# Performance work log

Hardware: AMD Instinct MI355X
Metric: run time of the kernel (lower is better)

Reference implementation:

```python
import jax, jax.numpy as jnp
import numpy as np

NQ = 4096
N0, N1 = 32768, 8192
N = N0 + N1
F = 128          # emb_dim (32x0e+32x1e)
H = 4            # num_heads
HD = F // H
NB = 64          # fc_neurons[0] radial basis size
DEG = 32
CUTOFFS = jnp.array([2.0, 4.0], dtype=jnp.float32)
OFFSETS = jnp.array([0.1, 0.2], dtype=jnp.float32)


def _sph_harm(u):
    # component-normalized real spherical harmonics l=0,1,2 of unit vectors u [E,3]
    x, y, z = u[:, 0], u[:, 1], u[:, 2]
    s3, s15, s5 = 3.0 ** 0.5, 15.0 ** 0.5, 5.0 ** 0.5
    return jnp.stack([
        jnp.ones_like(x),
        s3 * x, s3 * y, s3 * z,
        s15 * x * y, s15 * y * z, 0.5 * s5 * (3.0 * z * z - 1.0),
        s15 * x * z, 0.5 * s15 * (x * x - y * y),
    ], axis=-1)  # [E,9]


def setup_inputs() -> dict:
    key = jax.random.key(0)
    ks = jax.random.split(key, 20)
    E0 = NQ * DEG
    E1 = NQ * DEG
    edge_src = jnp.concatenate([
        jax.random.randint(ks[0], (E0,), 0, N0),
        jax.random.randint(ks[1], (E1,), N0, N),
    ])
    edge_dst = jnp.concatenate([
        jax.random.randint(ks[2], (E0,), 0, NQ),
        jax.random.randint(ks[3], (E1,), 0, NQ),
    ])
    scale_id = jnp.concatenate([jnp.zeros((E0,), jnp.int32), jnp.ones((E1,), jnp.int32)])
    r = lambda k, sh, s=1.0: jax.random.normal(k, sh, jnp.float32) * s
    return {
        'query_coord': r(ks[4], (NQ, 3)),
        'node_feature': r(ks[5], (N, F)),
        'node_coord': r(ks[6], (N, 3)),
        'edge_src': edge_src, 'edge_dst': edge_dst, 'scale_id': scale_id,
        'b_dst': r(ks[7], (F,)),
        'Wq': r(ks[8], (F, F), F ** -0.5),
        'Wk': r(ks[9], (F, F), F ** -0.5),
        'Wv': r(ks[10], (F, F), F ** -0.5),
        'Wo': r(ks[11], (F, F), F ** -0.5),
        'bo': r(ks[12], (F,)),
        'W_rad0': r(ks[13], (NB, NB), NB ** -0.5), 'b_rad0': r(ks[14], (NB,)),
        'W_rad1': r(ks[15], (NB, NB), NB ** -0.5), 'b_rad1': r(ks[16], (NB,)),
        'W_msg': r(ks[17], (NB, F), NB ** -0.5),
        'W_sh': r(ks[18], (9, F), 9 ** -0.5),
        'W_alpha': r(ks[19], (NB, H), NB ** -0.5),
    }


def _forward(query_coord, node_feature, node_coord, b_dst, Wq, Wk, Wv, Wo, bo,
             W_rad0, b_rad0, W_rad1, b_rad1, W_msg, W_sh, W_alpha,
             edge_src, edge_dst, scale_id):
    Nq = query_coord.shape[0]
    vec = node_coord[edge_src] - query_coord[edge_dst]            # [E,3]
    rlen = jnp.sqrt(jnp.sum(vec * vec, -1) + 1e-12)               # [E]
    off = OFFSETS[scale_id]
    cut = CUTOFFS[scale_id]
    xn = (rlen - off) / (cut - off)                               # normalized radius per scale
    centers = jnp.linspace(0.0, 1.0, NB)
    std = 1.0 / NB
    g = jnp.exp(-0.5 * ((xn[:, None] - centers) / std) ** 2)      # [E,NB] gaussian RBF
    soft = 0.5 * (1.0 + jnp.cos(jnp.pi * jnp.clip((xn - 0.8) / 0.2, 0.0, 1.0)))
    g = g * soft[:, None]                                         # soft finite cutoff
    # per-scale Linear after radial basis (2 scales, masked select)
    edge_scalar = jnp.where((scale_id == 0)[:, None], g @ W_rad0 + b_rad0, g @ W_rad1 + b_rad1)
    sh = _sph_harm(vec / rlen[:, None])                           # [E,9]
    # attention GNN (equiformer-style): dst features start as zeros + learned bias
    q = (b_dst @ Wq).reshape(H, HD)
    k = (node_feature @ Wk)[edge_src].reshape(-1, H, HD)
    logits = jnp.einsum('hd,ehd->eh', q, k) / (HD ** 0.5) + edge_scalar @ W_alpha  # [E,H]
    m = jax.ops.segment_max(logits, edge_dst, num_segments=Nq)
    p = jnp.exp(logits - m[edge_dst])
    denom = jax.ops.segment_sum(p, edge_dst, num_segments=Nq)
    alpha = p / (denom[edge_dst] + 1e-9)                          # segment softmax [E,H]
    v_e = (node_feature @ Wv)[edge_src] * (edge_scalar @ W_msg) + sh @ W_sh  # [E,F]
    msg = (alpha[:, :, None] * v_e.reshape(-1, H, HD)).reshape(-1, F)
    out = jax.ops.segment_sum(msg, edge_dst, num_segments=Nq)     # [Nq,F]
    return out @ Wo + bo


def reference(query_coord, node_feature, node_coord, edge_src, edge_dst, scale_id,
              b_dst, Wq, Wk, Wv, Wo, bo, W_rad0, b_rad0, W_rad1, b_rad1,
              W_msg, W_sh, W_alpha):
    return _forward(query_coord, node_feature, node_coord, b_dst, Wq, Wk, Wv, Wo, bo,
                    W_rad0, b_rad0, W_rad1, b_rad1, W_msg, W_sh, W_alpha,
                    edge_src, edge_dst, scale_id)
```

## Files before the change

### kernel.cpp

```cpp
#include <hip/hip_runtime.h>
#include <hip/hip_bf16.h>
#include <math.h>

#define PI_F 3.14159265358979323846f

typedef __attribute__((ext_vector_type(8))) short short8v;
typedef __attribute__((ext_vector_type(4))) float f32x4;

__device__ __forceinline__ short f2bf(float x) {
    return __builtin_bit_cast(short, __float2bfloat16(x));
}
__device__ __forceinline__ float bf2f(unsigned short u) {
    return __uint_as_float(((unsigned)u) << 16);
}
__device__ __forceinline__ int pack_bf2(float a, float b) {
    return (int)(unsigned short)f2bf(a) | ((int)(unsigned short)f2bf(b) << 16);
}

static const size_t WS_WA     = 0;
static const size_t WS_BA     = 512;
static const size_t WS_BM     = 520;
static const size_t WS_WMF    = 776;
static const size_t WS_WSHF   = 8968;
static const size_t WS_QKF    = 11016;
static const size_t WS_WVF    = 12040;
static const size_t WS_WOF    = 20232;
static const size_t WS_COUNTS = 28424;
static const size_t WS_OFFS   = 36624;
static const size_t WS_CURSOR = 44824;
static const size_t WS_PACKED = 53016;
static const size_t WS_LK     = 315160;
static const size_t WS_EDP    = 479000;
static const size_t WS_EDG    = 1527576;
static const size_t WS_VB     = 2576152;
static const size_t WS_OUTPRE = 5197592;

__global__ __launch_bounds__(256) void k_prepfmt(
    const float* b_dst, const float* Wq, const float* Wk,
    const float* W_rad0, const float* b_rad0,
    const float* W_rad1, const float* b_rad1,
    const float* W_msg, const float* W_alpha, const float* Wv,
    const float* Wo, const float* W_sh,
    const int* edge_dst, const int* scale_id,
    float* Wa, float* ba, float* bm,
    short* WmF, short* WshF, short* QKF, short* WVF, short* WOF,
    int* counts, int E, int NQr) {
    __shared__ float qs_s[128];
    __shared__ float qk_s[512];
    int t = threadIdx.x;
    int b = blockIdx.x;
    if (b == 0) {
        if (t < 128) {
            float acc = 0.f;
            for (int c = 0; c < 128; ++c) acc += b_dst[c] * Wq[c * 128 + t];
            qs_s[t] = acc;
        }
        __syncthreads();
        if (t < 128) {
            const float invs = 0.17677669529663687f;
            for (int h = 0; h < 4; ++h) {
                float acc = 0.f;
                for (int d = 0; d < 32; ++d)
                    acc += Wk[t * 128 + h * 32 + d] * qs_s[h * 32 + d];
                qk_s[t * 4 + h] = acc * invs;
            }
        }
        for (int idx = t; idx < 512; idx += 256) {
            int s = idx >> 8, i = (idx >> 2) & 63, h = idx & 3;
            const float* Wr = s ? W_rad1 : W_rad0;
            float acc = 0.f;
            for (int u = 0; u < 64; ++u) acc += Wr[i * 64 + u] * W_alpha[u * 4 + h];
            Wa[idx] = acc;
        }
        if (t < 8) {
            int s = t >> 2, h = t & 3;
            const float* br = s ? b_rad1 : b_rad0;
            float acc = 0.f;
            for (int u = 0; u < 64; ++u) acc += br[u] * W_alpha[u * 4 + h];
            ba[t] = acc;
        }
        {
            int s = t >> 7, c = t & 127;
            const float* br = s ? b_rad1 : b_rad0;
            float acc = 0.f;
            for (int u = 0; u < 64; ++u) acc += br[u] * W_msg[u * 128 + c];
            bm[t] = acc;
        }
        __syncthreads();
        for (int idx = t; idx < 2048; idx += 256) {
            int j = idx & 7, lane = (idx >> 3) & 63, kh = idx >> 9;
            int k = kh * 32 + ((lane >> 4) << 3) + j;
            int col = lane & 15;
            QKF[idx] = f2bf(col < 4 ? qk_s[k * 4 + col] : 0.f);
        }
    } else if (b <= 208) {
        int item = (b - 1) * 256 + t;
        if (item < 16384) {
            int j = item & 7, lane = (item >> 3) & 63, kh = (item >> 9) & 1;
            int ct = (item >> 10) & 7, sid = item >> 13;
            int k = kh * 32 + ((lane >> 4) << 3) + j;
            int c = (lane & 15) * 8 + ct;
            const float* Wr = sid ? W_rad1 : W_rad0;
            float acc = 0.f;
            for (int u = 0; u < 64; ++u) acc += Wr[k * 64 + u] * W_msg[u * 128 + c];
            WmF[item] = f2bf(acc);
        } else if (item < 20480) {
            int i2 = item - 16384;
            int j = i2 & 7, lane = (i2 >> 3) & 63, ct = (i2 >> 9) & 7;
            int k = ((lane >> 4) << 3) + j;
            int c = (lane & 15) * 8 + ct;
            WshF[i2] = f2bf(k < 9 ? W_sh[k * 128 + c] : 0.f);
        } else if (item < 36864) {
            int i2 = item - 20480;
            int j = i2 & 7, lane = (i2 >> 3) & 63, ct = (i2 >> 9) & 7, kh = (i2 >> 12) & 3;
            int k = kh * 32 + ((lane >> 4) << 3) + j;
            int c = (lane & 15) * 8 + ct;
            WVF[i2] = f2bf(Wv[k * 128 + c]);
        } else {
            int i2 = item - 36864;
            int j = i2 & 7, lane = (i2 >> 3) & 63, ct = (i2 >> 9) & 7, kh = (i2 >> 12) & 3;
            int k = kh * 32 + ((lane >> 4) << 3) + j;
            int c = (lane & 15) * 8 + ct;
            WOF[i2] = f2bf(Wo[k * 128 + c]);
        }
    } else {
        int e = (b - 209) * 256 + t;
        if (e < E) atomicAdd(&counts[scale_id[e] * NQr + edge_dst[e]], 1);
    }
}

template <typename OUT, bool LK>
__global__ __launch_bounds__(256) void k_mgemm(
    const float* A, const short* WF, const float* bias, OUT* out,
    float* lk, const short* QKF, int M) {
    int t = threadIdx.x;
    int w = t >> 6, lane = t & 63;
    int m = lane & 15, grp = lane >> 4;
    int row0 = (blockIdx.x * 4 + w) * 16;
    if (row0 >= M) return;

    short8v a[4];
#pragma unroll
    for (int kh = 0; kh < 4; ++kh) {
        const float* ap = &A[(size_t)(row0 + m) * 128 + kh * 32 + grp * 8];
        float4 f0 = *(const float4*)ap;
        float4 f1 = *(const float4*)(ap + 4);
        a[kh][0] = f2bf(f0.x); a[kh][1] = f2bf(f0.y);
        a[kh][2] = f2bf(f0.z); a[kh][3] = f2bf(f0.w);
        a[kh][4] = f2bf(f1.x); a[kh][5] = f2bf(f1.y);
        a[kh][6] = f2bf(f1.z); a[kh][7] = f2bf(f1.w);
    }
    if constexpr (LK) {
        f32x4 cl = {0.f, 0.f, 0.f, 0.f};
#pragma unroll
        for (int kh = 0; kh < 4; ++kh) {
            short8v qb = *(const short8v*)&QKF[(kh * 64 + lane) * 8];
            cl = __builtin_amdgcn_mfma_f32_16x16x32_bf16(a[kh], qb, cl, 0, 0, 0);
        }
        if (m < 4) {
#pragma unroll
            for (int r = 0; r < 4; ++r)
                lk[(size_t)(row0 + grp * 4 + r) * 4 + m] = cl[r];
        }
    }
    f32x4 c8[8];
#pragma unroll
    for (int ct = 0; ct < 8; ++ct) {
        f32x4 c = {0.f, 0.f, 0.f, 0.f};
#pragma unroll
        for (int kh = 0; kh < 4; ++kh) {
            short8v bf = *(const short8v*)&WF[((kh * 8 + ct) * 64 + lane) * 8];
            c = __builtin_amdgcn_mfma_f32_16x16x32_bf16(a[kh], bf, c, 0, 0, 0);
        }
        c8[ct] = c;
    }
    if constexpr (sizeof(OUT) == 2) {
#pragma unroll
        for (int r = 0; r < 4; ++r) {
            int row = row0 + grp * 4 + r;
            int4 sv;
            sv.x = pack_bf2(c8[0][r], c8[1][r]);
            sv.y = pack_bf2(c8[2][r], c8[3][r]);
            sv.z = pack_bf2(c8[4][r], c8[5][r]);
            sv.w = pack_bf2(c8[6][r], c8[7][r]);
            *(int4*)&out[(size_t)row * 128 + m * 8] = sv;
        }
    } else {
        float4 b0 = make_float4(0.f, 0.f, 0.f, 0.f), b1 = b0;
        if (bias) {
            b0 = *(const float4*)&bias[m * 8];
            b1 = *(const float4*)&bias[m * 8 + 4];
        }
#pragma unroll
        for (int r = 0; r < 4; ++r) {
            int row = row0 + grp * 4 + r;
            float4 o0 = make_float4(c8[0][r] + b0.x, c8[1][r] + b0.y,
                                    c8[2][r] + b0.z, c8[3][r] + b0.w);
            float4 o1 = make_float4(c8[4][r] + b1.x, c8[5][r] + b1.y,
                                    c8[6][r] + b1.z, c8[7][r] + b1.w);
            *(float4*)&out[(size_t)row * 128 + m * 8] = o0;
            *(float4*)&out[(size_t)row * 128 + m * 8 + 4] = o1;
        }
    }
}

__global__ void k_scan(const int* counts, int* offsets, int* cursor, int nkey) {
    __shared__ int sdata[256];
    int t = threadIdx.x;
    int chunk = (nkey + 255) / 256;
    int sum = 0;
    for (int i = 0; i < chunk; ++i) {
        int idx = t * chunk + i;
        sum += (idx < nkey) ? counts[idx] : 0;
    }
    sdata[t] = sum;
    __syncthreads();
    for (int off = 1; off < 256; off <<= 1) {
        int v = (t >= off) ? sdata[t - off] : 0;
        __syncthreads();
        sdata[t] += v;
        __syncthreads();
    }
    int run = sdata[t] - sum;
    for (int i = 0; i < chunk; ++i) {
        int idx = t * chunk + i;
        if (idx < nkey) {
            offsets[idx] = run;
            cursor[idx] = run;
            run += counts[idx];
        }
    }
    if (t == 255) offsets[nkey] = sdata[255];
}

__global__ __launch_bounds__(256) void k_scatter_edge(
    const int* edge_src, const int* edge_dst, const int* scale_id,
    const float* qc, const float* nc, const float* lk,
    const float* WaB, const float* baB, int* cursor,
    int* packed, float* edP, float* edG, int E, int NQr) {
    __shared__ float WaS[512];
    __shared__ float baS[8];
    int t = threadIdx.x;
    for (int i = t; i < 512; i += 256) WaS[i] = WaB[i];
    if (t < 8) baS[t] = baB[t];
    __syncthreads();
    int e = blockIdx.x * 256 + t;
    if (e >= E) return;
    int src = edge_src[e], dst = edge_dst[e], sid = scale_id[e];
    int pos = atomicAdd(&cursor[sid * NQr + dst], 1);

    float qx = qc[dst * 3 + 0], qy = qc[dst * 3 + 1], qz = qc[dst * 3 + 2];
    float vx = nc[src * 3 + 0] - qx;
    float vy = nc[src * 3 + 1] - qy;
    float vz = nc[src * 3 + 2] - qz;
    float r = sqrtf(vx * vx + vy * vy + vz * vz + 1e-12f);
    float rinv = 1.0f / r;
    float ux = vx * rinv, uy = vy * rinv, uz = vz * rinv;

    float roff = sid ? 0.2f : 0.1f;
    float rdiv = sid ? (1.0f / 3.8f) : (1.0f / 1.9f);
    float xn = (r - roff) * rdiv;
    float su = fminf(fmaxf((xn - 0.8f) * 5.0f, 0.0f), 1.0f);
    float soft = 0.5f * (1.0f + __cosf(PI_F * su));

    float4 lkv = *(const float4*)&lk[(size_t)src * 4];

    const float qs = 64.f / 63.f;
    const float Qc = __expf(-qs * qs);
    const float* Wrow = WaS + sid * 256;
    float a0 = 0.f, a1 = 0.f, a2 = 0.f, a3 = 0.f;
#pragma unroll
    for (int ch = 0; ch < 8; ++ch) {
        float d = (xn - (float)(ch * 8) * (1.0f / 63.0f)) * 64.0f;
        float g = __expf(-0.5f * d * d);
        float tt = __expf(fminf(qs * d - 0.5f * qs * qs, 60.f));
#pragma unroll
        for (int j = 0; j < 8; ++j) {
            float4 wa = *(const float4*)&Wrow[(ch * 8 + j) * 4];
            a0 = fmaf(g, wa.x, a0);
            a1 = fmaf(g, wa.y, a1);
            a2 = fmaf(g, wa.z, a2);
            a3 = fmaf(g, wa.w, a3);
            g *= tt; tt *= Qc;
        }
    }
    float p0 = __expf(lkv.x + soft * a0 + baS[sid * 4 + 0]);
    float p1 = __expf(lkv.y + soft * a1 + baS[sid * 4 + 1]);
    float p2 = __expf(lkv.z + soft * a2 + baS[sid * 4 + 2]);
    float p3 = __expf(lkv.w + soft * a3 + baS[sid * 4 + 3]);
    packed[pos] = src | (dst << 16);
    *(float4*)&edP[(size_t)pos * 4] = make_float4(p0, p1, p2, p3);
    *(float4*)&edG[(size_t)pos * 4] = make_float4(ux, uy, uz, xn);
}

__device__ __forceinline__ short8v gchain(float xn, int k0, float soft, float Qc) {
    const float qs = 64.f / 63.f;
    float d = (xn - (float)k0 * (1.0f / 63.0f)) * 64.0f;
    float g = __expf(-0.5f * d * d);
    float tt = __expf(fminf(qs * d - 0.5f * qs * qs, 60.f));
    short8v rr;
#pragma unroll
    for (int j = 0; j < 8; ++j) {
        rr[j] = f2bf(g * soft);
        g *= tt; tt *= Qc;
    }
    return rr;
}

__global__ __launch_bounds__(256) void k_main10(
    const int* offsets, const int* packed, const float* edP, const float* edG,
    const unsigned short* Vu, const float* bm, const short* WmF, const short* WshF,
    float* out_pre, int NQr) {
    __shared__ float part[4][132];
    int t = threadIdx.x;
    int w = t >> 6, lane = t & 63;
    int sid = w & 1;
    int dst = blockIdx.x * 2 + (w >> 1);
    int m = lane & 15, grp = lane >> 4;
    int h = m >> 2;

    int key = sid * NQr + dst;
    int s0 = offsets[key], s1 = offsets[key + 1];
    int nt = (s1 - s0 + 15) >> 4;

    float acc[8];
#pragma unroll
    for (int i = 0; i < 8; ++i) acc[i] = 0.f;
    float den = 0.f;

    float4 bm0 = *(const float4*)&bm[sid * 128 + m * 8];
    float4 bm1 = *(const float4*)&bm[sid * 128 + m * 8 + 4];
    float bmv[8] = {bm0.x, bm0.y, bm0.z, bm0.w, bm1.x, bm1.y, bm1.z, bm1.w};
    const short* wmp = WmF + sid * 8192;

    const float qs = 64.f / 63.f;
    const float Qc = __expf(-qs * qs);
    const float s3 = 1.7320508075688772f, s15 = 3.872983346207417f, s5 = 2.23606797749979f;

    if (nt > 0) {
        auto loadA = [&](int tl, int (&srcs)[4], float (&ph)[4], float4& G4) {
            int q0 = s0 + tl * 16;
            int posA = q0 + m; if (posA >= s1) posA = s1 - 1;
            G4 = *(const float4*)&edG[(size_t)posA * 4];
#pragma unroll
            for (int r = 0; r < 4; ++r) {
                int pos = q0 + grp * 4 + r;
                bool valid = pos < s1;
                if (!valid) pos = s1 - 1;
                srcs[r] = packed[pos] & 0xFFFF;
                float p = edP[(size_t)pos * 4 + h];
                ph[r] = valid ? p : 0.f;
            }
        };
        auto loadV = [&](const int (&srcs)[4], int4 (&vv)[4]) {
#pragma unroll
            for (int r = 0; r < 4; ++r)
                vv[r] = *(const int4*)&Vu[(size_t)srcs[r] * 128 + m * 8];
        };

        int srcsA[4], srcsB[4], srcsC[4];
        float phA[4], phB[4], phC[4];
        float4 gA, gB, gC;
        int4 vA[4], vB[4];

        loadA(0, srcsA, phA, gA);
        loadV(srcsA, vA);
        if (nt > 1) loadA(1, srcsB, phB, gB);

        for (int tl = 0; tl < nt; ++tl) {
            if (tl + 1 < nt) loadV(srcsB, vB);
            if (tl + 2 < nt) loadA(tl + 2, srcsC, phC, gC);

            int wds[4][4];
#pragma unroll
            for (int r = 0; r < 4; ++r) {
                wds[r][0] = vA[r].x; wds[r][1] = vA[r].y;
                wds[r][2] = vA[r].z; wds[r][3] = vA[r].w;
            }
            den += phA[0] + phA[1] + phA[2] + phA[3];

            float xn = gA.w;
            float su = fminf(fmaxf((xn - 0.8f) * 5.0f, 0.0f), 1.0f);
            float soft = 0.5f * (1.0f + __cosf(PI_F * su));
            short8v aG0 = gchain(xn, grp * 8, soft, Qc);
            short8v aG1 = gchain(xn, 32 + grp * 8, soft, Qc);

            float ux = gA.x, uy = gA.y, uz = gA.z;
            float sh[9];
            sh[0] = 1.f; sh[1] = s3 * ux; sh[2] = s3 * uy; sh[3] = s3 * uz;
            sh[4] = s15 * ux * uy; sh[5] = s15 * uy * uz;
            sh[6] = 0.5f * s5 * (3.f * uz * uz - 1.f);
            sh[7] = s15 * ux * uz; sh[8] = 0.5f * s15 * (ux * ux - uy * uy);
            short8v aS;
#pragma unroll
            for (int j = 0; j < 8; ++j) {
                float v = (grp == 0) ? sh[j] : ((grp == 1 && j == 0) ? sh[8] : 0.f);
                aS[j] = f2bf(v);
            }

#pragma unroll
            for (int ct = 0; ct < 8; ++ct) {
                short8v b0 = *(const short8v*)&wmp[((ct * 2 + 0) * 64 + lane) * 8];
                short8v b1 = *(const short8v*)&wmp[((ct * 2 + 1) * 64 + lane) * 8];
                short8v bS = *(const short8v*)&WshF[(ct * 64 + lane) * 8];
                f32x4 cms = {bmv[ct], bmv[ct], bmv[ct], bmv[ct]};
                cms = __builtin_amdgcn_mfma_f32_16x16x32_bf16(aG0, b0, cms, 0, 0, 0);
                cms = __builtin_amdgcn_mfma_f32_16x16x32_bf16(aG1, b1, cms, 0, 0, 0);
                f32x4 csh = {0.f, 0.f, 0.f, 0.f};
                csh = __builtin_amdgcn_mfma_f32_16x16x32_bf16(aS, bS, csh, 0, 0, 0);
#pragma unroll
                for (int r = 0; r < 4; ++r) {
                    int wd = wds[r][ct >> 1];
                    unsigned short vu = (ct & 1) ? (unsigned short)(wd >> 16)
                                                 : (unsigned short)(wd & 0xFFFF);
                    float vf = bf2f(vu);
                    float ve = fmaf(vf, cms[r], csh[r]);
                    acc[ct] = fmaf(phA[r], ve, acc[ct]);
                }
            }

            gA = gB; gB = gC;
#pragma unroll
            for (int r = 0; r < 4; ++r) {
                phA[r] = phB[r]; phB[r] = phC[r];
                srcsB[r] = srcsC[r];
                vA[r] = vB[r];
            }
        }
    }

#pragma unroll
    for (int i = 0; i < 8; ++i) {
        acc[i] += __shfl_xor(acc[i], 16);
        acc[i] += __shfl_xor(acc[i], 32);
    }
    den += __shfl_xor(den, 16);
    den += __shfl_xor(den, 32);
    if (lane < 16) {
#pragma unroll
        for (int ct = 0; ct < 8; ++ct) part[w][m * 8 + ct] = acc[ct];
        if ((m & 3) == 0) part[w][128 + h] = den;
    }
    __syncthreads();

    {
        int which = t >> 7;
        int col = t & 127;
        int d2 = blockIdx.x * 2 + which;
        if (d2 < NQr) {
            int hh = col >> 5;
            float s = part[2 * which][col] + part[2 * which + 1][col];
            float d = part[2 * which][128 + hh] + part[2 * which + 1][128 + hh];
            out_pre[(size_t)d2 * 128 + col] = s / (d + 1e-9f);
        }
    }
}

extern "C" void kernel_launch(void* const* d_in, const int* in_sizes, int n_in,
                              void* d_out, int out_size, void* d_ws, size_t ws_size,
                              hipStream_t stream) {
    const float* query_coord = (const float*)d_in[0];
    const float* node_feature = (const float*)d_in[1];
    const float* node_coord = (const float*)d_in[2];
    const int* edge_src = (const int*)d_in[3];
    const int* edge_dst = (const int*)d_in[4];
    const int* scale_id = (const int*)d_in[5];
    const float* b_dst = (const float*)d_in[6];
    const float* Wq = (const float*)d_in[7];
    const float* Wk = (const float*)d_in[8];
    const float* Wv = (const float*)d_in[9];
    const float* Wo = (const float*)d_in[10];
    const float* bo = (const float*)d_in[11];
    const float* W_rad0 = (const float*)d_in[12];
    const float* b_rad0 = (const float*)d_in[13];
    const float* W_rad1 = (const float*)d_in[14];
    const float* b_rad1 = (const float*)d_in[15];
    const float* W_msg = (const float*)d_in[16];
    const float* W_sh = (const float*)d_in[17];
    const float* W_alpha = (const float*)d_in[18];
    (void)n_in; (void)ws_size; (void)out_size;

    int NQr = in_sizes[0] / 3;
    int Nn = in_sizes[1] / 128;
    int E = in_sizes[3];
    int nkey = NQr * 2;

    float* ws = (float*)d_ws;
    float* Wa = ws + WS_WA;
    float* ba = ws + WS_BA;
    float* bm = ws + WS_BM;
    short* WmF = (short*)(ws + WS_WMF);
    short* WshF = (short*)(ws + WS_WSHF);
    short* QKF = (short*)(ws + WS_QKF);
    short* WVF = (short*)(ws + WS_WVF);
    short* WOF = (short*)(ws + WS_WOF);
    int* counts = (int*)(ws + WS_COUNTS);
    int* offsets = (int*)(ws + WS_OFFS);
    int* cursor = (int*)(ws + WS_CURSOR);
    int* packed = (int*)(ws + WS_PACKED);
    float* lk = ws + WS_LK;
    float* edP = ws + WS_EDP;
    float* edG = ws + WS_EDG;
    unsigned short* Vb = (unsigned short*)(ws + WS_VB);
    float* out_pre = ws + WS_OUTPRE;
    float* out = (float*)d_out;

    hipMemsetAsync(counts, 0, nkey * sizeof(int), stream);
    int histBlocks = (E + 255) / 256;
    hipLaunchKernelGGL(k_prepfmt, dim3(209 + histBlocks), dim3(256), 0, stream,
                       b_dst, Wq, Wk, W_rad0, b_rad0, W_rad1, b_rad1, W_msg, W_alpha,
                       Wv, Wo, W_sh, edge_dst, scale_id,
                       Wa, ba, bm, WmF, WshF, QKF, WVF, WOF, counts, E, NQr);
    hipLaunchKernelGGL((k_mgemm<unsigned short, true>), dim3((Nn + 63) / 64), dim3(256), 0,
                       stream, node_feature, WVF, (const float*)nullptr, Vb, lk, QKF, Nn);
    hipLaunchKernelGGL(k_scan, dim3(1), dim3(256), 0, stream, counts, offsets, cursor, nkey);
    hipLaunchKernelGGL(k_scatter_edge, dim3((E + 255) / 256), dim3(256), 0, stream,
                       edge_src, edge_dst, scale_id, query_coord, node_coord, lk,
                       Wa, ba, cursor, packed, edP, edG, E, NQr);
    hipLaunchKernelGGL(k_main10, dim3((NQr + 1) / 2), dim3(256), 0, stream,
                       offsets, packed, edP, edG, Vb, bm, WmF, WshF, out_pre, NQr);
    hipLaunchKernelGGL((k_mgemm<float, false>), dim3((NQr + 63) / 64), dim3(256), 0, stream,
                       out_pre, WOF, bo, out, (float*)nullptr, (const short*)nullptr, NQr);
}
```

Baseline: 129.7 us.

## Fuse edge geometry and attention logits into main kernel via MFMA

Result: slower. 148.4 us (+14.5%).

```diff
diff --git a/kernel.cpp b/kernel.cpp
--- a/kernel.cpp
+++ b/kernel.cpp
@@ -17,7 +17,6 @@
     return (int)(unsigned short)f2bf(a) | ((int)(unsigned short)f2bf(b) << 16);
 }
 
-static const size_t WS_WA     = 0;
 static const size_t WS_BA     = 512;
 static const size_t WS_BM     = 520;
 static const size_t WS_WMF    = 776;
@@ -25,15 +24,14 @@
 static const size_t WS_QKF    = 11016;
 static const size_t WS_WVF    = 12040;
 static const size_t WS_WOF    = 20232;
-static const size_t WS_COUNTS = 28424;
-static const size_t WS_OFFS   = 36624;
-static const size_t WS_CURSOR = 44824;
-static const size_t WS_PACKED = 53016;
-static const size_t WS_LK     = 315160;
-static const size_t WS_EDP    = 479000;
-static const size_t WS_EDG    = 1527576;
-static const size_t WS_VB     = 2576152;
-static const size_t WS_OUTPRE = 5197592;
+static const size_t WS_WAF    = 28424;
+static const size_t WS_COUNTS = 29448;
+static const size_t WS_OFFS   = 37640;
+static const size_t WS_CURSOR = 45840;
+static const size_t WS_PACKED = 54032;
+static const size_t WS_LK     = 316176;
+static const size_t WS_VB     = 480016;
+static const size_t WS_OUTPRE = 3101456;
 
 __global__ __launch_bounds__(256) void k_prepfmt(
     const float* b_dst, const float* Wq, const float* Wk,
@@ -42,11 +40,12 @@
     const float* W_msg, const float* W_alpha, const float* Wv,
     const float* Wo, const float* W_sh,
     const int* edge_dst, const int* scale_id,
-    float* Wa, float* ba, float* bm,
-    short* WmF, short* WshF, short* QKF, short* WVF, short* WOF,
+    float* ba, float* bm,
+    short* WmF, short* WshF, short* QKF, short* WVF, short* WOF, short* WaF,
     int* counts, int E, int NQr) {
     __shared__ float qs_s[128];
     __shared__ float qk_s[512];
+    __shared__ float wa_s[512];
     int t = threadIdx.x;
     int b = blockIdx.x;
     if (b == 0) {
@@ -70,7 +69,7 @@
             const float* Wr = s ? W_rad1 : W_rad0;
             float acc = 0.f;
             for (int u = 0; u < 64; ++u) acc += Wr[i * 64 + u] * W_alpha[u * 4 + h];
-            Wa[idx] = acc;
+            wa_s[idx] = acc;
         }
         if (t < 8) {
             int s = t >> 2, h = t & 3;
@@ -92,6 +91,12 @@
             int k = kh * 32 + ((lane >> 4) << 3) + j;
             int col = lane & 15;
             QKF[idx] = f2bf(col < 4 ? qk_s[k * 4 + col] : 0.f);
+        }
+        for (int idx = t; idx < 2048; idx += 256) {
+            int j = idx & 7, lane = (idx >> 3) & 63, kh = (idx >> 9) & 1, sid = idx >> 10;
+            int k = kh * 32 + ((lane >> 4) << 3) + j;
+            int col = lane & 15;
+            WaF[idx] = f2bf(col < 4 ? wa_s[sid * 256 + k * 4 + col] : 0.f);
         }
     } else if (b <= 208) {
         int item = (b - 1) * 256 + t;
@@ -233,64 +238,14 @@
     if (t == 255) offsets[nkey] = sdata[255];
 }
 
-__global__ __launch_bounds__(256) void k_scatter_edge(
-    const int* edge_src, const int* edge_dst, const int* scale_id,
-    const float* qc, const float* nc, const float* lk,
-    const float* WaB, const float* baB, int* cursor,
-    int* packed, float* edP, float* edG, int E, int NQr) {
-    __shared__ float WaS[512];
-    __shared__ float baS[8];
-    int t = threadIdx.x;
-    for (int i = t; i < 512; i += 256) WaS[i] = WaB[i];
-    if (t < 8) baS[t] = baB[t];
-    __syncthreads();
-    int e = blockIdx.x * 256 + t;
-    if (e >= E) return;
-    int src = edge_src[e], dst = edge_dst[e], sid = scale_id[e];
-    int pos = atomicAdd(&cursor[sid * NQr + dst], 1);
-
-    float qx = qc[dst * 3 + 0], qy = qc[dst * 3 + 1], qz = qc[dst * 3 + 2];
-    float vx = nc[src * 3 + 0] - qx;
-    float vy = nc[src * 3 + 1] - qy;
-    float vz = nc[src * 3 + 2] - qz;
-    float r = sqrtf(vx * vx + vy * vy + vz * vz + 1e-12f);
-    float rinv = 1.0f / r;
-    float ux = vx * rinv, uy = vy * rinv, uz = vz * rinv;
-
-    float roff = sid ? 0.2f : 0.1f;
-    float rdiv = sid ? (1.0f / 3.8f) : (1.0f / 1.9f);
-    float xn = (r - roff) * rdiv;
-    float su = fminf(fmaxf((xn - 0.8f) * 5.0f, 0.0f), 1.0f);
-    float soft = 0.5f * (1.0f + __cosf(PI_F * su));
-
-    float4 lkv = *(const float4*)&lk[(size_t)src * 4];
-
-    const float qs = 64.f / 63.f;
-    const float Qc = __expf(-qs * qs);
-    const float* Wrow = WaS + sid * 256;
-    float a0 = 0.f, a1 = 0.f, a2 = 0.f, a3 = 0.f;
-#pragma unroll
-    for (int ch = 0; ch < 8; ++ch) {
-        float d = (xn - (float)(ch * 8) * (1.0f / 63.0f)) * 64.0f;
-        float g = __expf(-0.5f * d * d);
-        float tt = __expf(fminf(qs * d - 0.5f * qs * qs, 60.f));
-#pragma unroll
-        for (int j = 0; j < 8; ++j) {
-            float4 wa = *(const float4*)&Wrow[(ch * 8 + j) * 4];
-            a0 = fmaf(g, wa.x, a0);
-            a1 = fmaf(g, wa.y, a1);
-            a2 = fmaf(g, wa.z, a2);
-            a3 = fmaf(g, wa.w, a3);
-            g *= tt; tt *= Qc;
-        }
-    }
-    float p0 = __expf(lkv.x + soft * a0 + baS[sid * 4 + 0]);
-    float p1 = __expf(lkv.y + soft * a1 + baS[sid * 4 + 1]);
-    float p2 = __expf(lkv.z + soft * a2 + baS[sid * 4 + 2]);
-    float p3 = __expf(lkv.w + soft * a3 + baS[sid * 4 + 3]);
-    packed[pos] = src | (dst << 16);
-    *(float4*)&edP[(size_t)pos * 4] = make_float4(p0, p1, p2, p3);
-    *(float4*)&edG[(size_t)pos * 4] = make_float4(ux, uy, uz, xn);
+__global__ void k_scatter(const int* edge_src, const int* edge_dst, const int* scale_id,
+                          int* cursor, int* packed, int E, int NQr) {
+    int e = blockIdx.x * 256 + threadIdx.x;
+    if (e < E) {
+        int dst = edge_dst[e];
+        int pos = atomicAdd(&cursor[scale_id[e] * NQr + dst], 1);
+        packed[pos] = edge_src[e] | (dst << 16);
+    }
 }
 
 __device__ __forceinline__ short8v gchain(float xn, int k0, float soft, float Qc) {
@@ -307,9 +262,11 @@
     return rr;
 }
 
-__global__ __launch_bounds__(256) void k_main10(
-    const int* offsets, const int* packed, const float* edP, const float* edG,
-    const unsigned short* Vu, const float* bm, const short* WmF, const short* WshF,
+__global__ __launch_bounds__(256) void k_main11(
+    const int* offsets, const int* packed, const float* lk,
+    const float* qc, const float* nc,
+    const unsigned short* Vu, const float* bm, const float* baB,
+    const short* WmF, const short* WshF, const short* WaF,
     float* out_pre, int NQr) {
     __shared__ float part[4][132];
     int t = threadIdx.x;
@@ -328,64 +285,63 @@
     for (int i = 0; i < 8; ++i) acc[i] = 0.f;
     float den = 0.f;
 
+    float qx = qc[dst * 3 + 0], qy = qc[dst * 3 + 1], qz = qc[dst * 3 + 2];
+    float bav = baB[sid * 4 + h];
     float4 bm0 = *(const float4*)&bm[sid * 128 + m * 8];
     float4 bm1 = *(const float4*)&bm[sid * 128 + m * 8 + 4];
     float bmv[8] = {bm0.x, bm0.y, bm0.z, bm0.w, bm1.x, bm1.y, bm1.z, bm1.w};
     const short* wmp = WmF + sid * 8192;
-
+    const short* wap = WaF + sid * 1024;
+
+    float roff = sid ? 0.2f : 0.1f;
+    float rdiv = sid ? (1.0f / 3.8f) : (1.0f / 1.9f);
     const float qs = 64.f / 63.f;
     const float Qc = __expf(-qs * qs);
     const float s3 = 1.7320508075688772f, s15 = 3.872983346207417f, s5 = 2.23606797749979f;
 
     if (nt > 0) {
-        auto loadA = [&](int tl, int (&srcs)[4], float (&ph)[4], float4& G4) {
+        auto loadPK = [&](int tl) -> int {
+            int pos = s0 + tl * 16 + m;
+            if (pos >= s1) pos = s1 - 1;
+            return packed[pos];
+        };
+        auto issue = [&](int pk, float (&ncv)[3], float (&lkv)[4], int4 (&vv)[4]) {
+            int mySrc = pk & 0xFFFF;
+            ncv[0] = nc[mySrc * 3 + 0];
+            ncv[1] = nc[mySrc * 3 + 1];
+            ncv[2] = nc[mySrc * 3 + 2];
+#pragma unroll
+            for (int r = 0; r < 4; ++r) {
+                int s = __shfl(mySrc, grp * 4 + r);
+                lkv[r] = lk[(size_t)s * 4 + h];
+                vv[r] = *(const int4*)&Vu[(size_t)s * 128 + m * 8];
+            }
+        };
+
+        int pkA, pkB = 0, pkC = 0;
+        float ncA[3], ncB[3];
+        float lkA[4], lkB[4];
+        int4 vA[4], vB[4];
+
+        pkA = loadPK(0);
+        issue(pkA, ncA, lkA, vA);
+        if (nt > 1) pkB = loadPK(1);
+
+        for (int tl = 0; tl < nt; ++tl) {
+            if (tl + 1 < nt) issue(pkB, ncB, lkB, vB);
+            if (tl + 2 < nt) pkC = loadPK(tl + 2);
+
             int q0 = s0 + tl * 16;
-            int posA = q0 + m; if (posA >= s1) posA = s1 - 1;
-            G4 = *(const float4*)&edG[(size_t)posA * 4];
-#pragma unroll
-            for (int r = 0; r < 4; ++r) {
-                int pos = q0 + grp * 4 + r;
-                bool valid = pos < s1;
-                if (!valid) pos = s1 - 1;
-                srcs[r] = packed[pos] & 0xFFFF;
-                float p = edP[(size_t)pos * 4 + h];
-                ph[r] = valid ? p : 0.f;
-            }
-        };
-        auto loadV = [&](const int (&srcs)[4], int4 (&vv)[4]) {
-#pragma unroll
-            for (int r = 0; r < 4; ++r)
-                vv[r] = *(const int4*)&Vu[(size_t)srcs[r] * 128 + m * 8];
-        };
-
-        int srcsA[4], srcsB[4], srcsC[4];
-        float phA[4], phB[4], phC[4];
-        float4 gA, gB, gC;
-        int4 vA[4], vB[4];
-
-        loadA(0, srcsA, phA, gA);
-        loadV(srcsA, vA);
-        if (nt > 1) loadA(1, srcsB, phB, gB);
-
-        for (int tl = 0; tl < nt; ++tl) {
-            if (tl + 1 < nt) loadV(srcsB, vB);
-            if (tl + 2 < nt) loadA(tl + 2, srcsC, phC, gC);
-
-            int wds[4][4];
-#pragma unroll
-            for (int r = 0; r < 4; ++r) {
-                wds[r][0] = vA[r].x; wds[r][1] = vA[r].y;
-                wds[r][2] = vA[r].z; wds[r][3] = vA[r].w;
-            }
-            den += phA[0] + phA[1] + phA[2] + phA[3];
-
-            float xn = gA.w;
+            float vx = ncA[0] - qx, vy = ncA[1] - qy, vz = ncA[2] - qz;
+            float rr = sqrtf(vx * vx + vy * vy + vz * vz + 1e-12f);
+            float rinv = 1.0f / rr;
+            float ux = vx * rinv, uy = vy * rinv, uz = vz * rinv;
+            float xn = (rr - roff) * rdiv;
             float su = fminf(fmaxf((xn - 0.8f) * 5.0f, 0.0f), 1.0f);
             float soft = 0.5f * (1.0f + __cosf(PI_F * su));
             short8v aG0 = gchain(xn, grp * 8, soft, Qc);
             short8v aG1 = gchain(xn, 32 + grp * 8, soft, Qc);
 
-            float ux = gA.x, uy = gA.y, uz = gA.z;
             float sh[9];
             sh[0] = 1.f; sh[1] = s3 * ux; sh[2] = s3 * uy; sh[3] = s3 * uz;
             sh[4] = s15 * ux * uy; sh[5] = s15 * uy * uz;
@@ -396,6 +352,28 @@
             for (int j = 0; j < 8; ++j) {
                 float v = (grp == 0) ? sh[j] : ((grp == 1 && j == 0) ? sh[8] : 0.f);
                 aS[j] = f2bf(v);
+            }
+
+            short8v wa0 = *(const short8v*)&wap[(0 * 64 + lane) * 8];
+            short8v wa1 = *(const short8v*)&wap[(1 * 64 + lane) * 8];
+            f32x4 cal = {0.f, 0.f, 0.f, 0.f};
+            cal = __builtin_amdgcn_mfma_f32_16x16x32_bf16(aG0, wa0, cal, 0, 0, 0);
+            cal = __builtin_amdgcn_mfma_f32_16x16x32_bf16(aG1, wa1, cal, 0, 0, 0);
+
+            float ph[4];
+#pragma unroll
+            for (int r = 0; r < 4; ++r) {
+                float av = __shfl(cal[r], (lane & 48) | h);
+                bool valid = (q0 + grp * 4 + r) < s1;
+                ph[r] = valid ? __expf(lkA[r] + av + bav) : 0.f;
+            }
+            den += ph[0] + ph[1] + ph[2] + ph[3];
+
+            int wds[4][4];
+#pragma unroll
+            for (int r = 0; r < 4; ++r) {
+                wds[r][0] = vA[r].x; wds[r][1] = vA[r].y;
+                wds[r][2] = vA[r].z; wds[r][3] = vA[r].w;
             }
 
 #pragma unroll
@@ -415,17 +393,14 @@
                                                  : (unsigned short)(wd & 0xFFFF);
                     float vf = bf2f(vu);
                     float ve = fmaf(vf, cms[r], csh[r]);
-                    acc[ct] = fmaf(phA[r], ve, acc[ct]);
+                    acc[ct] = fmaf(ph[r], ve, acc[ct]);
                 }
             }
 
-            gA = gB; gB = gC;
-#pragma unroll
-            for (int r = 0; r < 4; ++r) {
-                phA[r] = phB[r]; phB[r] = phC[r];
-                srcsB[r] = srcsC[r];
-                vA[r] = vB[r];
-            }
+            ncA[0] = ncB[0]; ncA[1] = ncB[1]; ncA[2] = ncB[2];
+#pragma unroll
+            for (int r = 0; r < 4; ++r) { lkA[r] = lkB[r]; vA[r] = vB[r]; }
+            pkB = pkC;
         }
     }
 
@@ -486,7 +461,6 @@
     int nkey = NQr * 2;
 
     float* ws = (float*)d_ws;
-    float* Wa = ws + WS_WA;
     float* ba = ws + WS_BA;
     float* bm = ws + WS_BM;
     short* WmF = (short*)(ws + WS_WMF);
@@ -494,13 +468,12 @@
     short* QKF = (short*)(ws + WS_QKF);
     short* WVF = (short*)(ws + WS_WVF);
     short* WOF = (short*)(ws + WS_WOF);
+    short* WaF = (short*)(ws + WS_WAF);
     int* counts = (int*)(ws + WS_COUNTS);
     int* offsets = (int*)(ws + WS_OFFS);
     int* cursor = (int*)(ws + WS_CURSOR);
     int* packed = (int*)(ws + WS_PACKED);
     float* lk = ws + WS_LK;
-    float* edP = ws + WS_EDP;
-    float* edG = ws + WS_EDG;
     unsigned short* Vb = (unsigned short*)(ws + WS_VB);
     float* out_pre = ws + WS_OUTPRE;
     float* out = (float*)d_out;
@@ -510,15 +483,15 @@
     hipLaunchKernelGGL(k_prepfmt, dim3(209 + histBlocks), dim3(256), 0, stream,
                        b_dst, Wq, Wk, W_rad0, b_rad0, W_rad1, b_rad1, W_msg, W_alpha,
                        Wv, Wo, W_sh, edge_dst, scale_id,
-                       Wa, ba, bm, WmF, WshF, QKF, WVF, WOF, counts, E, NQr);
+                       ba, bm, WmF, WshF, QKF, WVF, WOF, WaF, counts, E, NQr);
     hipLaunchKernelGGL((k_mgemm<unsigned short, true>), dim3((Nn + 63) / 64), dim3(256), 0,
                        stream, node_feature, WVF, (const float*)nullptr, Vb, lk, QKF, Nn);
     hipLaunchKernelGGL(k_scan, dim3(1), dim3(256), 0, stream, counts, offsets, cursor, nkey);
-    hipLaunchKernelGGL(k_scatter_edge, dim3((E + 255) / 256), dim3(256), 0, stream,
-                       edge_src, edge_dst, scale_id, query_coord, node_coord, lk,
-                       Wa, ba, cursor, packed, edP, edG, E, NQr);
-    hipLaunchKernelGGL(k_main10, dim3((NQr + 1) / 2), dim3(256), 0, stream,
-                       offsets, packed, edP, edG, Vb, bm, WmF, WshF, out_pre, NQr);
+    hipLaunchKernelGGL(k_scatter, dim3((E + 255) / 256), dim3(256), 0, stream,
+                       edge_src, edge_dst, scale_id, cursor, packed, E, NQr);
+    hipLaunchKernelGGL(k_main11, dim3((NQr + 1) / 2), dim3(256), 0, stream,
+                       offsets, packed, lk, query_coord, node_coord, Vb, bm, ba,
+                       WmF, WshF, WaF, out_pre, NQr);
     hipLaunchKernelGGL((k_mgemm<float, false>), dim3((NQr + 63) / 64), dim3(256), 0, stream,
                        out_pre, WOF, bo, out, (float*)nullptr, (const short*)nullptr, NQr);
 }
```
